# Performance work log

Measured on AMD Instinct MI355X. Metric: run time of the kernel, lower is better.

The kernel has to match this reference:

```python
import jax, jax.numpy as jnp
import numpy as np

EPS = 1e-5
NEG = -1e22

def layernorm(x, g, b):
    m = jnp.mean(x, axis=-1, keepdims=True)
    v = jnp.mean((x - m) ** 2, axis=-1, keepdims=True)
    return (x - m) * jax.lax.rsqrt(v + EPS) * g + b

def setup_inputs() -> dict:
    key = jax.random.key(0)
    ks = jax.random.split(key, 16)
    B, N, D, K = 4, 2048, 512, 32
    H = int(D * 1.5)  # 768
    sc = lambda fan_in: 1.0 / np.sqrt(fan_in)
    inp = {
        'x': jax.random.normal(ks[0], (B, N, D), jnp.float32),
        'adj': jax.random.uniform(ks[1], (B, N, N), jnp.float32),
        'inxs': jax.random.randint(ks[2], (B, N, K), 0, N, jnp.int64),
        'Wq': jax.random.normal(ks[3], (D, D), jnp.float32) * sc(D),
        'bq': jnp.zeros((D,), jnp.float32),
        'Wk': jax.random.normal(ks[4], (D, D), jnp.float32) * sc(D),
        'bk': jnp.zeros((D,), jnp.float32),
        'Wv': jax.random.normal(ks[5], (D, D), jnp.float32) * sc(D),
        'bv': jnp.zeros((D,), jnp.float32),
        'Wo': jax.random.normal(ks[6], (D, D), jnp.float32) * sc(D),
        'bo': jnp.zeros((D,), jnp.float32),
        'g1': jnp.ones((D,), jnp.float32),
        'beta1': jnp.zeros((D,), jnp.float32),
        'W1': jax.random.normal(ks[7], (D, H), jnp.float32) * sc(D),
        'bf1': jnp.zeros((H,), jnp.float32),
        'W2': jax.random.normal(ks[8], (H, D), jnp.float32) * sc(H),
        'bf2': jnp.zeros((D,), jnp.float32),
        'g2': jnp.ones((D,), jnp.float32),
        'beta2': jnp.zeros((D,), jnp.float32),
    }
    return inp

def reference(x, adj, inxs, Wq, bq, Wk, bk, Wv, bv, Wo, bo, g1, beta1, W1, bf1, W2, bf2, g2, beta2):
    B, N, D = x.shape
    # projections
    q = x @ Wq + bq                                   # [B,N,D]
    k = x @ Wk + bk
    v = x @ Wv + bv
    # gather top-k neighbor keys/values: [B,N,K,D]
    b_idx = jnp.arange(B)[:, None, None]
    k_nei = k[b_idx, inxs]
    v_nei = v[b_idx, inxs]
    # attention over selected neighbors, masked by adjacency sign
    scores = jnp.einsum('bnd,bnkd->bnk', q, k_nei) / jnp.sqrt(jnp.float32(D))
    adj_nei = jnp.take_along_axis(adj, inxs, axis=2)  # [B,N,K]
    mask = jnp.where(adj_nei > 0, 0.0, NEG)
    attn = jax.nn.softmax(scores + mask, axis=-1)
    att_out = jnp.einsum('bnk,bnkd->bnd', attn, v_nei) @ Wo + bo
    # residual + LN
    y = layernorm(x + jax.nn.relu(att_out), g1, beta1)
    # FFN + residual + LN
    h = jax.nn.relu(y @ W1 + bf1) @ W2 + bf2
    return layernorm(y + h, g2, beta2)
```

## Files before the change

kernel.cpp:

```cpp
#include <hip/hip_runtime.h>
#include <stdint.h>

typedef __attribute__((ext_vector_type(8))) short short8;
typedef __attribute__((ext_vector_type(4))) float f32x4;
typedef __attribute__((ext_vector_type(2))) _Float16 h2;
typedef __attribute__((ext_vector_type(8))) _Float16 half8;

static __device__ __forceinline__ unsigned short f2bf(float f) {
  unsigned int u = __float_as_uint(f);
  u += 0x7FFFu + ((u >> 16) & 1u);
  return (unsigned short)(u >> 16);
}
static __device__ __forceinline__ float bf2f(unsigned short h) {
  return __uint_as_float(((unsigned int)h) << 16);
}
static __device__ __forceinline__ unsigned short f2h(float f) {
  _Float16 h = (_Float16)f;
  return __builtin_bit_cast(unsigned short, h);
}
static __device__ __forceinline__ float hdot2(unsigned int a, unsigned int b, float c) {
  return __builtin_amdgcn_fdot2(__builtin_bit_cast(h2, a), __builtin_bit_cast(h2, b), c, false);
}

#define GLD16(gp, lp) __builtin_amdgcn_global_load_lds( \
    (__attribute__((address_space(1))) void*)(gp), \
    (__attribute__((address_space(3))) void*)(lp), 16, 0, 0)

__global__ __launch_bounds__(256) void k_cvt(const float* __restrict__ in,
                                             unsigned short* __restrict__ out) {
  const int bid = blockIdx.x;
  const int xcd = bid & 7;
  const int bb = xcd >> 1;
  const int s = ((bid >> 3) << 1) | (xcd & 1);
  const long row = ((long)bb << 11) | ((long)s << 2) | (threadIdx.x >> 6);
  const int lane = threadIdx.x & 63;
  const float4* p = (const float4*)(in + row * 512 + lane * 8);
  float4 a = p[0], b = p[1];
  short8 v;
  v[0] = (short)f2h(a.x); v[1] = (short)f2h(a.y);
  v[2] = (short)f2h(a.z); v[3] = (short)f2h(a.w);
  v[4] = (short)f2h(b.x); v[5] = (short)f2h(b.y);
  v[6] = (short)f2h(b.z); v[7] = (short)f2h(b.w);
  *(short8*)(out + row * 512 + lane * 8) = v;
}

__global__ __launch_bounds__(256) void k_mask(const float* __restrict__ adj,
                                              const int* __restrict__ inxs,
                                              float* __restrict__ maskb) {
  const int bid = blockIdx.x;
  const int xcd = bid & 7;
  const int bb = xcd >> 1;
  const int s = ((bid >> 3) << 1) | (xcd & 1);
  const long row = ((long)bb << 11) | ((long)s << 3) | (threadIdx.x >> 5);
  const int kk = threadIdx.x & 31;
  const int idx = inxs[row * 32 + kk];
  const float a = adj[row * 2048 + idx];
  maskb[row * 32 + kk] = a > 0.f ? 0.f : -1e22f;
}

__global__ __launch_bounds__(256) void k_tpose_all(
    const float* __restrict__ Wq, const float* __restrict__ Wk,
    const float* __restrict__ Wv, const float* __restrict__ Wo,
    const float* __restrict__ W1, const float* __restrict__ W2,
    unsigned short* __restrict__ wqkvt, unsigned short* __restrict__ wot,
    unsigned short* __restrict__ w1t, unsigned short* __restrict__ w2t) {
  __shared__ float tile[32][33];
  const int bid = blockIdx.x;
  const float* src;
  unsigned short* dst;
  int R, C, f16, local;
  if (bid < 768) {
    const int m = bid >> 8;
    src = m == 0 ? Wq : (m == 1 ? Wk : Wv);
    dst = wqkvt + (long)m * 512 * 512;
    R = 512; C = 512; f16 = 1; local = bid & 255;
  } else if (bid < 1024) {
    src = Wo; dst = wot; R = 512; C = 512; f16 = 0; local = bid - 768;
  } else if (bid < 1408) {
    src = W1; dst = w1t; R = 512; C = 768; f16 = 0; local = bid - 1024;
  } else {
    src = W2; dst = w2t; R = 768; C = 512; f16 = 0; local = bid - 1408;
  }
  const int ntx = C >> 5;
  const int c0 = (local % ntx) << 5;
  const int r0 = (local / ntx) << 5;
  const int tx = threadIdx.x, ty = threadIdx.y;
#pragma unroll
  for (int i = 0; i < 4; i++)
    tile[ty + i * 8][tx] = src[(long)(r0 + ty + i * 8) * C + c0 + tx];
  __syncthreads();
#pragma unroll
  for (int i = 0; i < 4; i++) {
    float v = tile[tx][ty + i * 8];
    dst[(long)(c0 + ty + i * 8) * R + r0 + tx] = f16 ? f2h(v) : f2bf(v);
  }
}

template <int EPI, int F16, int QKVB>
__global__ __launch_bounds__(256) void k_gemm(const unsigned short* __restrict__ A,
                                              const unsigned short* __restrict__ Bt,
                                              const float* __restrict__ bias,
                                              const float* __restrict__ bias2,
                                              const float* __restrict__ bias3,
                                              unsigned short* __restrict__ C,
                                              int M, int N, int K) {
  __shared__ unsigned short As[2][128 * 64];
  __shared__ unsigned short Bs[2][64 * 64];
  const int t = threadIdx.x;
  const int lane = t & 63;
  const int w = t >> 6;
  const int wr = w >> 1, wc = w & 1;
  const int lin = blockIdx.x;
  const int xcd = lin & 7;
  const int bb = xcd >> 1;
  const int nx = N >> 6;
  const int s = ((lin >> 3) << 1) | (xcd & 1);
  const int m0 = (bb * 16 + s / nx) * 128;
  const int n0 = (s % nx) * 64;

  f32x4 acc[4][2];
#pragma unroll
  for (int mi = 0; mi < 4; mi++)
#pragma unroll
    for (int ni = 0; ni < 2; ni++) {
      f32x4 z = {0.f, 0.f, 0.f, 0.f};
      acc[mi][ni] = z;
    }

  auto stage = [&](int buf, int k0) {
#pragma unroll
    for (int i = 0; i < 4; i++) {
      const int c = t + i * 256;
      const int r = c >> 3, j = c & 7;
      GLD16(A + (long)(m0 + r) * K + k0 + ((j ^ (r & 7)) << 3), &As[buf][c * 8]);
    }
#pragma unroll
    for (int i = 0; i < 2; i++) {
      const int c = t + i * 256;
      const int r = c >> 3, j = c & 7;
      GLD16(Bt + (long)(n0 + r) * K + k0 + ((j ^ (r & 7)) << 3), &Bs[buf][c * 8]);
    }
  };

  const int nt = K >> 6;
  stage(0, 0);
  for (int tt = 0; tt < nt; ++tt) {
    const int cur = tt & 1;
    if (tt + 1 < nt) {
      stage(cur ^ 1, (tt + 1) << 6);
      asm volatile("s_waitcnt vmcnt(6)" ::: "memory");
    } else {
      asm volatile("s_waitcnt vmcnt(0)" ::: "memory");
    }
    __builtin_amdgcn_s_barrier();

#pragma unroll
    for (int kk = 0; kk < 2; kk++) {
      short8 af[4], bf[2];
#pragma unroll
      for (int mi = 0; mi < 4; mi++) {
        const int r = wr * 64 + mi * 16 + (lane & 15);
        const int jj = (kk << 2) + (lane >> 4);
        af[mi] = *(const short8*)&As[cur][r * 64 + ((jj ^ (r & 7)) << 3)];
      }
#pragma unroll
      for (int ni = 0; ni < 2; ni++) {
        const int r = wc * 32 + ni * 16 + (lane & 15);
        const int jj = (kk << 2) + (lane >> 4);
        bf[ni] = *(const short8*)&Bs[cur][r * 64 + ((jj ^ (r & 7)) << 3)];
      }
#pragma unroll
      for (int mi = 0; mi < 4; mi++)
#pragma unroll
        for (int ni = 0; ni < 2; ni++) {
          if (F16)
            acc[mi][ni] = __builtin_amdgcn_mfma_f32_16x16x32_f16(
                __builtin_bit_cast(half8, af[mi]), __builtin_bit_cast(half8, bf[ni]),
                acc[mi][ni], 0, 0, 0);
          else
            acc[mi][ni] = __builtin_amdgcn_mfma_f32_16x16x32_bf16(af[mi], bf[ni], acc[mi][ni], 0, 0, 0);
        }
    }
    asm volatile("s_waitcnt lgkmcnt(0)" ::: "memory");
    __builtin_amdgcn_s_barrier();
  }

  const int lr = (lane >> 4) * 4;
  const int lc = lane & 15;
#pragma unroll
  for (int mi = 0; mi < 4; mi++) {
#pragma unroll
    for (int ni = 0; ni < 2; ni++) {
      const int col = n0 + wc * 32 + ni * 16 + lc;
      float bv;
      if (QKVB)
        bv = col < 512 ? bias[col] : (col < 1024 ? bias2[col - 512] : bias3[col - 1024]);
      else
        bv = bias[col];
#pragma unroll
      for (int r = 0; r < 4; r++) {
        const int row = m0 + wr * 64 + mi * 16 + lr + r;
        float v = acc[mi][ni][r] + bv;
        if (EPI == 1) v = fmaxf(v, 0.f);
        C[(long)row * N + col] = F16 ? f2h(v) : f2bf(v);
      }
    }
  }
}

__global__ __launch_bounds__(256) void k_attn(const unsigned short* __restrict__ qkv,
                                              const float* __restrict__ maskb,
                                              const int* __restrict__ inxs,
                                              unsigned short* __restrict__ att) {
  const int t = threadIdx.x;
  const int lane = t & 63;
  const int w = t >> 6;
  const int bid = blockIdx.x;
  const int xcd = bid & 7;
  const int b = xcd >> 1;
  const int sub = ((bid >> 3) << 1) | (xcd & 1);
  const int row = (b << 11) | (sub << 2) | w;
  const long base = (long)b * 2048;
  const int g = lane >> 4;
  const int li = lane & 15;
  const int kk = lane & 31;

  const int* ix = inxs + (long)row * 32;
  const int ixv = ix[kk];
  const float mval = maskb[(long)row * 32 + kk];

  const uint4* qp = (const uint4*)(qkv + (long)row * 1536);
  uint4 qc[4];
#pragma unroll
  for (int c = 0; c < 4; c++) qc[c] = qp[li + c * 16];

  float scr[8];
  uint4 ka[4], kb[4];
  {
    const int nb = __shfl(ixv, g, 64);
    const uint4* kp = (const uint4*)(qkv + (base + nb) * 1536 + 512);
#pragma unroll
    for (int c = 0; c < 4; c++) ka[c] = kp[li + c * 16];
  }
#pragma unroll
  for (int r = 0; r < 8; r++) {
    uint4* curk = (r & 1) ? kb : ka;
    uint4* nxtk = (r & 1) ? ka : kb;
    if (r < 7) {
      const int nb = __shfl(ixv, (r + 1) * 4 + g, 64);
      const uint4* kp = (const uint4*)(qkv + (base + nb) * 1536 + 512);
#pragma unroll
      for (int c = 0; c < 4; c++) nxtk[c] = kp[li + c * 16];
    }
    float d = 0.f;
#pragma unroll
    for (int c = 0; c < 4; c++) {
      d = hdot2(curk[c].x, qc[c].x, d);
      d = hdot2(curk[c].y, qc[c].y, d);
      d = hdot2(curk[c].z, qc[c].z, d);
      d = hdot2(curk[c].w, qc[c].w, d);
    }
#pragma unroll
    for (int m = 1; m <= 8; m <<= 1) d += __shfl_xor(d, m, 64);
    scr[r] = d;
  }

  const int srcl = (kk & 3) << 4;
  float s = __shfl(scr[0], srcl, 64);
#pragma unroll
  for (int r = 1; r < 8; r++) {
    const float tr = __shfl(scr[r], srcl, 64);
    s = ((kk >> 2) == r) ? tr : s;
  }
  s = s * 0.044194173824159216f + mval;

  float mx = s;
#pragma unroll
  for (int d = 1; d <= 16; d <<= 1) mx = fmaxf(mx, __shfl_xor(mx, d, 64));
  const float e = __expf(s - mx);
  float ts = e;
#pragma unroll
  for (int d = 1; d <= 16; d <<= 1) ts += __shfl_xor(ts, d, 64);
  const float inv = 1.f / ts;

  float o[8] = {0, 0, 0, 0, 0, 0, 0, 0};
  uint4 va0, va1, vb0, vb1;
  {
    const int u0 = __shfl(ixv, 0, 64);
    const int u1 = __shfl(ixv, 1, 64);
    va0 = *(const uint4*)(qkv + (base + u0) * 1536 + 1024 + lane * 8);
    va1 = *(const uint4*)(qkv + (base + u1) * 1536 + 1024 + lane * 8);
  }
#pragma unroll
  for (int p = 0; p < 16; p++) {
    const uint4 v0c = (p & 1) ? vb0 : va0;
    const uint4 v1c = (p & 1) ? vb1 : va1;
    if (p < 15) {
      const int u0 = __shfl(ixv, 2 * p + 2, 64);
      const int u1 = __shfl(ixv, 2 * p + 3, 64);
      const uint4 n0 = *(const uint4*)(qkv + (base + u0) * 1536 + 1024 + lane * 8);
      const uint4 n1 = *(const uint4*)(qkv + (base + u1) * 1536 + 1024 + lane * 8);
      if (p & 1) { va0 = n0; va1 = n1; } else { vb0 = n0; vb1 = n1; }
    }
    const float pe0 = __shfl(e, 2 * p, 64);
    const float pe1 = __shfl(e, 2 * p + 1, 64);
    const unsigned int pp =
        __builtin_bit_cast(unsigned int, __builtin_amdgcn_cvt_pkrtz(pe0, pe1));
    const unsigned int vw0[4] = {v0c.x, v0c.y, v0c.z, v0c.w};
    const unsigned int vw1[4] = {v1c.x, v1c.y, v1c.z, v1c.w};
#pragma unroll
    for (int q = 0; q < 4; q++) {
      const unsigned int even = __builtin_amdgcn_perm(vw1[q], vw0[q], 0x05040100u);
      const unsigned int odd  = __builtin_amdgcn_perm(vw1[q], vw0[q], 0x07060302u);
      o[2 * q]     = hdot2(even, pp, o[2 * q]);
      o[2 * q + 1] = hdot2(odd,  pp, o[2 * q + 1]);
    }
  }

  short8 ov;
#pragma unroll
  for (int j = 0; j < 8; j++) ov[j] = (short)f2bf(o[j] * inv);
  *(short8*)(att + (long)row * 512 + lane * 8) = ov;
}

__global__ __launch_bounds__(256) void k_ln1(const float* __restrict__ x,
                                             const unsigned short* __restrict__ o,
                                             const float* __restrict__ g,
                                             const float* __restrict__ beta,
                                             unsigned short* __restrict__ y) {
  const int lane = threadIdx.x & 63;
  const int w = threadIdx.x >> 6;
  const int bid = blockIdx.x;
  const int xcd = bid & 7;
  const int bb = xcd >> 1;
  const int s0 = ((bid >> 3) << 1) | (xcd & 1);
  const long row = ((long)bb << 11) | ((long)s0 << 2) | w;
  const float4* xp = (const float4*)(x + row * 512 + lane * 8);
  float4 x0 = xp[0], x1 = xp[1];
  short8 ov = *(const short8*)(o + row * 512 + lane * 8);
  float tv[8] = {x0.x, x0.y, x0.z, x0.w, x1.x, x1.y, x1.z, x1.w};
  float s = 0.f, s2 = 0.f;
#pragma unroll
  for (int j = 0; j < 8; j++) {
    tv[j] += bf2f((unsigned short)ov[j]);
    s += tv[j];
    s2 += tv[j] * tv[j];
  }
#pragma unroll
  for (int m = 32; m >= 1; m >>= 1) {
    s += __shfl_xor(s, m, 64);
    s2 += __shfl_xor(s2, m, 64);
  }
  const float mean = s * (1.f / 512.f);
  const float var = s2 * (1.f / 512.f) - mean * mean;
  const float r = rsqrtf(var + 1e-5f);
  const float4* gp = (const float4*)(g + lane * 8);
  const float4* bp = (const float4*)(beta + lane * 8);
  float4 g0 = gp[0], g1v = gp[1], b0 = bp[0], b1 = bp[1];
  float gg[8] = {g0.x, g0.y, g0.z, g0.w, g1v.x, g1v.y, g1v.z, g1v.w};
  float bb2[8] = {b0.x, b0.y, b0.z, b0.w, b1.x, b1.y, b1.z, b1.w};
  short8 yv;
#pragma unroll
  for (int j = 0; j < 8; j++) yv[j] = (short)f2bf((tv[j] - mean) * r * gg[j] + bb2[j]);
  *(short8*)(y + row * 512 + lane * 8) = yv;
}

__global__ __launch_bounds__(256) void k_ln2(const unsigned short* __restrict__ y,
                                             const unsigned short* __restrict__ f,
                                             const float* __restrict__ g,
                                             const float* __restrict__ beta,
                                             float* __restrict__ out) {
  const int lane = threadIdx.x & 63;
  const int w = threadIdx.x >> 6;
  const int bid = blockIdx.x;
  const int xcd = bid & 7;
  const int bb = xcd >> 1;
  const int s0 = ((bid >> 3) << 1) | (xcd & 1);
  const long row = ((long)bb << 11) | ((long)s0 << 2) | w;
  short8 yv = *(const short8*)(y + row * 512 + lane * 8);
  short8 fv = *(const short8*)(f + row * 512 + lane * 8);
  float tv[8];
  float s = 0.f, s2 = 0.f;
#pragma unroll
  for (int j = 0; j < 8; j++) {
    tv[j] = bf2f((unsigned short)yv[j]) + bf2f((unsigned short)fv[j]);
    s += tv[j];
    s2 += tv[j] * tv[j];
  }
#pragma unroll
  for (int m = 32; m >= 1; m >>= 1) {
    s += __shfl_xor(s, m, 64);
    s2 += __shfl_xor(s2, m, 64);
  }
  const float mean = s * (1.f / 512.f);
  const float var = s2 * (1.f / 512.f) - mean * mean;
  const float r = rsqrtf(var + 1e-5f);
  const float4* gp = (const float4*)(g + lane * 8);
  const float4* bp = (const float4*)(beta + lane * 8);
  float4 g0 = gp[0], g1v = gp[1], b0 = bp[0], b1 = bp[1];
  float gg[8] = {g0.x, g0.y, g0.z, g0.w, g1v.x, g1v.y, g1v.z, g1v.w};
  float bb2[8] = {b0.x, b0.y, b0.z, b0.w, b1.x, b1.y, b1.z, b1.w};
  float ovv[8];
#pragma unroll
  for (int j = 0; j < 8; j++) ovv[j] = (tv[j] - mean) * r * gg[j] + bb2[j];
  float4* op = (float4*)(out + row * 512 + lane * 8);
  float4 o0 = {ovv[0], ovv[1], ovv[2], ovv[3]};
  float4 o1 = {ovv[4], ovv[5], ovv[6], ovv[7]};
  op[0] = o0;
  op[1] = o1;
}

extern "C" void kernel_launch(void* const* d_in, const int* in_sizes, int n_in,
                              void* d_out, int out_size, void* d_ws, size_t ws_size,
                              hipStream_t stream) {
  const float* x   = (const float*)d_in[0];
  const float* adj = (const float*)d_in[1];
  const int*   inx = (const int*)d_in[2];
  const float* Wq  = (const float*)d_in[3];
  const float* bq  = (const float*)d_in[4];
  const float* Wk  = (const float*)d_in[5];
  const float* bk  = (const float*)d_in[6];
  const float* Wv  = (const float*)d_in[7];
  const float* bv  = (const float*)d_in[8];
  const float* Wo  = (const float*)d_in[9];
  const float* bo  = (const float*)d_in[10];
  const float* g1  = (const float*)d_in[11];
  const float* be1 = (const float*)d_in[12];
  const float* W1  = (const float*)d_in[13];
  const float* bf1 = (const float*)d_in[14];
  const float* W2  = (const float*)d_in[15];
  const float* bf2 = (const float*)d_in[16];
  const float* g2  = (const float*)d_in[17];
  const float* be2 = (const float*)d_in[18];

  unsigned short* xb    = (unsigned short*)d_ws;
  unsigned short* wqkvt = xb + 4194304;
  unsigned short* wot   = wqkvt + 786432;
  unsigned short* w1t   = wot + 262144;
  unsigned short* w2t   = w1t + 393216;
  unsigned short* qkv   = w2t + 393216;
  unsigned short* oproj = qkv + 12582912;
  unsigned short* y     = oproj + 4194304;
  float*          maskb = (float*)(y + 4194304);
  unsigned short* att   = xb;
  unsigned short* h     = qkv;
  unsigned short* f     = oproj;

  k_mask<<<1024, 256, 0, stream>>>(adj, inx, maskb);
  k_cvt<<<2048, 256, 0, stream>>>(x, xb);
  k_tpose_all<<<1792, dim3(32, 8), 0, stream>>>(Wq, Wk, Wv, Wo, W1, W2,
                                                wqkvt, wot, w1t, w2t);

  k_gemm<0, 1, 1><<<1536, 256, 0, stream>>>(xb, wqkvt, bq, bk, bv, qkv, 8192, 1536, 512);
  k_attn<<<2048, 256, 0, stream>>>(qkv, maskb, inx, att);
  k_gemm<1, 0, 0><<<512, 256, 0, stream>>>(att, wot, bo, bo, bo, oproj, 8192, 512, 512);
  k_ln1<<<2048, 256, 0, stream>>>(x, oproj, g1, be1, y);
  k_gemm<1, 0, 0><<<768, 256, 0, stream>>>(y, w1t, bf1, bf1, bf1, h, 8192, 768, 512);
  k_gemm<0, 0, 0><<<512, 256, 0, stream>>>(h, w2t, bf2, bf2, bf2, f, 8192, 512, 768);
  k_ln2<<<2048, 256, 0, stream>>>(y, f, g2, be2, (float*)d_out);
}
```

Before: 115.9 us.

## Merge prep kernels into one launch and simplify attention gather for occupancy

Three preprocessing kernels (mask build, x fp16 conversion, weight transposes) are merged into one k_prep launch that dispatches on block index, removing two launches and their inter-kernel gaps. Separately, the attention kernel drops its manual double-buffered K/V prefetch registers and adds a min-blocks launch bound of 8, aiming for lower register use and higher occupancy so the hardware hides gather latency instead. The risk is losing explicit load/compute overlap if the compiler does not schedule loads early enough.

```diff
diff --git a/kernel.cpp b/kernel.cpp
--- a/kernel.cpp
+++ b/kernel.cpp
@@ -26,39 +26,10 @@
     (__attribute__((address_space(1))) void*)(gp), \
     (__attribute__((address_space(3))) void*)(lp), 16, 0, 0)
 
-__global__ __launch_bounds__(256) void k_cvt(const float* __restrict__ in,
-                                             unsigned short* __restrict__ out) {
-  const int bid = blockIdx.x;
-  const int xcd = bid & 7;
-  const int bb = xcd >> 1;
-  const int s = ((bid >> 3) << 1) | (xcd & 1);
-  const long row = ((long)bb << 11) | ((long)s << 2) | (threadIdx.x >> 6);
-  const int lane = threadIdx.x & 63;
-  const float4* p = (const float4*)(in + row * 512 + lane * 8);
-  float4 a = p[0], b = p[1];
-  short8 v;
-  v[0] = (short)f2h(a.x); v[1] = (short)f2h(a.y);
-  v[2] = (short)f2h(a.z); v[3] = (short)f2h(a.w);
-  v[4] = (short)f2h(b.x); v[5] = (short)f2h(b.y);
-  v[6] = (short)f2h(b.z); v[7] = (short)f2h(b.w);
-  *(short8*)(out + row * 512 + lane * 8) = v;
-}
-
-__global__ __launch_bounds__(256) void k_mask(const float* __restrict__ adj,
-                                              const int* __restrict__ inxs,
-                                              float* __restrict__ maskb) {
-  const int bid = blockIdx.x;
-  const int xcd = bid & 7;
-  const int bb = xcd >> 1;
-  const int s = ((bid >> 3) << 1) | (xcd & 1);
-  const long row = ((long)bb << 11) | ((long)s << 3) | (threadIdx.x >> 5);
-  const int kk = threadIdx.x & 31;
-  const int idx = inxs[row * 32 + kk];
-  const float a = adj[row * 2048 + idx];
-  maskb[row * 32 + kk] = a > 0.f ? 0.f : -1e22f;
-}
-
-__global__ __launch_bounds__(256) void k_tpose_all(
+__global__ __launch_bounds__(256) void k_prep(
+    const float* __restrict__ adj, const int* __restrict__ inxs,
+    float* __restrict__ maskb, const float* __restrict__ x,
+    unsigned short* __restrict__ xb,
     const float* __restrict__ Wq, const float* __restrict__ Wk,
     const float* __restrict__ Wv, const float* __restrict__ Wo,
     const float* __restrict__ W1, const float* __restrict__ W2,
@@ -66,25 +37,55 @@
     unsigned short* __restrict__ w1t, unsigned short* __restrict__ w2t) {
   __shared__ float tile[32][33];
   const int bid = blockIdx.x;
+  const int t = threadIdx.x;
+  if (bid < 1024) {
+    const int xcd = bid & 7;
+    const int bb = xcd >> 1;
+    const int s = ((bid >> 3) << 1) | (xcd & 1);
+    const long row = ((long)bb << 11) | ((long)s << 3) | (t >> 5);
+    const int kk = t & 31;
+    const int idx = inxs[row * 32 + kk];
+    const float a = adj[row * 2048 + idx];
+    maskb[row * 32 + kk] = a > 0.f ? 0.f : -1e22f;
+    return;
+  }
+  if (bid < 3072) {
+    const int lb = bid - 1024;
+    const int xcd = lb & 7;
+    const int bb = xcd >> 1;
+    const int s = ((lb >> 3) << 1) | (xcd & 1);
+    const long row = ((long)bb << 11) | ((long)s << 2) | (t >> 6);
+    const int lane = t & 63;
+    const float4* p = (const float4*)(x + row * 512 + lane * 8);
+    float4 a = p[0], b = p[1];
+    short8 v;
+    v[0] = (short)f2h(a.x); v[1] = (short)f2h(a.y);
+    v[2] = (short)f2h(a.z); v[3] = (short)f2h(a.w);
+    v[4] = (short)f2h(b.x); v[5] = (short)f2h(b.y);
+    v[6] = (short)f2h(b.z); v[7] = (short)f2h(b.w);
+    *(short8*)(xb + row * 512 + lane * 8) = v;
+    return;
+  }
+  const int lb = bid - 3072;
   const float* src;
   unsigned short* dst;
   int R, C, f16, local;
-  if (bid < 768) {
-    const int m = bid >> 8;
+  if (lb < 768) {
+    const int m = lb >> 8;
     src = m == 0 ? Wq : (m == 1 ? Wk : Wv);
     dst = wqkvt + (long)m * 512 * 512;
-    R = 512; C = 512; f16 = 1; local = bid & 255;
-  } else if (bid < 1024) {
-    src = Wo; dst = wot; R = 512; C = 512; f16 = 0; local = bid - 768;
-  } else if (bid < 1408) {
-    src = W1; dst = w1t; R = 512; C = 768; f16 = 0; local = bid - 1024;
+    R = 512; C = 512; f16 = 1; local = lb & 255;
+  } else if (lb < 1024) {
+    src = Wo; dst = wot; R = 512; C = 512; f16 = 0; local = lb - 768;
+  } else if (lb < 1408) {
+    src = W1; dst = w1t; R = 512; C = 768; f16 = 0; local = lb - 1024;
   } else {
-    src = W2; dst = w2t; R = 768; C = 512; f16 = 0; local = bid - 1408;
+    src = W2; dst = w2t; R = 768; C = 512; f16 = 0; local = lb - 1408;
   }
   const int ntx = C >> 5;
   const int c0 = (local % ntx) << 5;
   const int r0 = (local / ntx) << 5;
-  const int tx = threadIdx.x, ty = threadIdx.y;
+  const int tx = t & 31, ty = t >> 5;
 #pragma unroll
   for (int i = 0; i < 4; i++)
     tile[ty + i * 8][tx] = src[(long)(r0 + ty + i * 8) * C + c0 + tx];
@@ -208,10 +209,10 @@
   }
 }
 
-__global__ __launch_bounds__(256) void k_attn(const unsigned short* __restrict__ qkv,
-                                              const float* __restrict__ maskb,
-                                              const int* __restrict__ inxs,
-                                              unsigned short* __restrict__ att) {
+__global__ __launch_bounds__(256, 8) void k_attn(const unsigned short* __restrict__ qkv,
+                                                 const float* __restrict__ maskb,
+                                                 const int* __restrict__ inxs,
+                                                 unsigned short* __restrict__ att) {
   const int t = threadIdx.x;
   const int lane = t & 63;
   const int w = t >> 6;
@@ -235,30 +236,18 @@
   for (int c = 0; c < 4; c++) qc[c] = qp[li + c * 16];
 
   float scr[8];
-  uint4 ka[4], kb[4];
-  {
-    const int nb = __shfl(ixv, g, 64);
+#pragma unroll
+  for (int r = 0; r < 8; r++) {
+    const int nb = __shfl(ixv, r * 4 + g, 64);
     const uint4* kp = (const uint4*)(qkv + (base + nb) * 1536 + 512);
-#pragma unroll
-    for (int c = 0; c < 4; c++) ka[c] = kp[li + c * 16];
-  }
-#pragma unroll
-  for (int r = 0; r < 8; r++) {
-    uint4* curk = (r & 1) ? kb : ka;
-    uint4* nxtk = (r & 1) ? ka : kb;
-    if (r < 7) {
-      const int nb = __shfl(ixv, (r + 1) * 4 + g, 64);
-      const uint4* kp = (const uint4*)(qkv + (base + nb) * 1536 + 512);
-#pragma unroll
-      for (int c = 0; c < 4; c++) nxtk[c] = kp[li + c * 16];
-    }
     float d = 0.f;
 #pragma unroll
     for (int c = 0; c < 4; c++) {
-      d = hdot2(curk[c].x, qc[c].x, d);
-      d = hdot2(curk[c].y, qc[c].y, d);
-      d = hdot2(curk[c].z, qc[c].z, d);
-      d = hdot2(curk[c].w, qc[c].w, d);
+      uint4 kc = kp[li + c * 16];
+      d = hdot2(kc.x, qc[c].x, d);
+      d = hdot2(kc.y, qc[c].y, d);
+      d = hdot2(kc.z, qc[c].z, d);
+      d = hdot2(kc.w, qc[c].w, d);
     }
 #pragma unroll
     for (int m = 1; m <= 8; m <<= 1) d += __shfl_xor(d, m, 64);
@@ -284,24 +273,12 @@
   const float inv = 1.f / ts;
 
   float o[8] = {0, 0, 0, 0, 0, 0, 0, 0};
-  uint4 va0, va1, vb0, vb1;
-  {
-    const int u0 = __shfl(ixv, 0, 64);
-    const int u1 = __shfl(ixv, 1, 64);
-    va0 = *(const uint4*)(qkv + (base + u0) * 1536 + 1024 + lane * 8);
-    va1 = *(const uint4*)(qkv + (base + u1) * 1536 + 1024 + lane * 8);
-  }
 #pragma unroll
   for (int p = 0; p < 16; p++) {
-    const uint4 v0c = (p & 1) ? vb0 : va0;
-    const uint4 v1c = (p & 1) ? vb1 : va1;
-    if (p < 15) {
-      const int u0 = __shfl(ixv, 2 * p + 2, 64);
-      const int u1 = __shfl(ixv, 2 * p + 3, 64);
-      const uint4 n0 = *(const uint4*)(qkv + (base + u0) * 1536 + 1024 + lane * 8);
-      const uint4 n1 = *(const uint4*)(qkv + (base + u1) * 1536 + 1024 + lane * 8);
-      if (p & 1) { va0 = n0; va1 = n1; } else { vb0 = n0; vb1 = n1; }
-    }
+    const int u0 = __shfl(ixv, 2 * p, 64);
+    const int u1 = __shfl(ixv, 2 * p + 1, 64);
+    const uint4 v0c = *(const uint4*)(qkv + (base + u0) * 1536 + 1024 + lane * 8);
+    const uint4 v1c = *(const uint4*)(qkv + (base + u1) * 1536 + 1024 + lane * 8);
     const float pe0 = __shfl(e, 2 * p, 64);
     const float pe1 = __shfl(e, 2 * p + 1, 64);
     const unsigned int pp =
@@ -446,10 +423,8 @@
   unsigned short* h     = qkv;
   unsigned short* f     = oproj;
 
-  k_mask<<<1024, 256, 0, stream>>>(adj, inx, maskb);
-  k_cvt<<<2048, 256, 0, stream>>>(x, xb);
-  k_tpose_all<<<1792, dim3(32, 8), 0, stream>>>(Wq, Wk, Wv, Wo, W1, W2,
-                                                wqkvt, wot, w1t, w2t);
+  k_prep<<<4864, 256, 0, stream>>>(adj, inx, maskb, x, xb, Wq, Wk, Wv, Wo, W1, W2,
+                                   wqkvt, wot, w1t, w2t);
 
   k_gemm<0, 1, 1><<<1536, 256, 0, stream>>>(xb, wqkvt, bq, bk, bv, qkv, 8192, 1536, 512);
   k_attn<<<2048, 256, 0, stream>>>(qkv, maskb, inx, att);
```

New measurement: 114.5 us. Within noise of the previous version (-1.2%).
